# Performance work log

Measured on AMD Instinct MI355X. Metric: run time of the kernel, lower is better.

The kernel has to match this reference:

```python
import jax, jax.numpy as jnp
import numpy as np

STRIDE = (1, 2, 2, 1)

def setup_inputs() -> dict:
    key = jax.random.key(0)
    k1, k2 = jax.random.split(key)
    B, H, W, C = 8, 128, 128, 64
    out_flat = (H * STRIDE[1]) * (W * STRIDE[2]) * C  # 4194304
    inputs = jax.random.normal(k1, (B, H, W, C), dtype=jnp.float32)
    indices = jax.random.randint(k2, (B, H, W, C), 0, out_flat, dtype=jnp.int64)
    return {"inputs": inputs, "indices": indices}

def reference(inputs, indices):
    # Max-unpooling: scatter pooled values into a (stride_h*H, stride_w*W) map
    # using per-batch flat argmax indices. tf.scatter_nd sums duplicates -> .add
    B, H, W, C = inputs.shape
    oH, oW = H * STRIDE[1], W * STRIDE[2]
    flat_out = oH * oW * C
    pool_flat = inputs.reshape(B, H * W * C)
    ind_flat = indices.reshape(B, H * W * C)
    b = jnp.arange(B, dtype=ind_flat.dtype)[:, None]  # [B,1] batch index
    ret = jnp.zeros((B, flat_out), dtype=inputs.dtype)
    ret = ret.at[jnp.broadcast_to(b, ind_flat.shape), ind_flat].add(pool_flat)
    return ret.reshape(B, oH, oW, C)
```

## Files before the change

### kernel.cpp

```cpp
#include <hip/hip_runtime.h>


typedef unsigned int u32;
typedef float nat_f4 __attribute__((ext_vector_type(4)));

constexpr int N             = 1 << 23;
constexpr int NBINS         = 4096;
constexpr int BINS_PER_B    = 512;
constexpr int BIN_FLOATS    = 8192;
constexpr int CAP           = 3072;
constexpr int KA_BLOCKS     = 1024;
constexpr int PAIRS_PER_BLK = 8192;
constexpr size_t SLAB_BYTES = (size_t)NBINS * CAP * 8;
constexpr size_t WS_NEEDED  = SLAB_BYTES + (size_t)NBINS * 4;

__global__ __launch_bounds__(512, 4) void kA_sort(const int4* __restrict__ idx4,
                                                  const float4* __restrict__ val4,
                                                  uint2* __restrict__ slab,
                                                  u32* __restrict__ cursor) {
    __shared__ u32 lhist[BINS_PER_B];
    __shared__ u32 lstart[BINS_PER_B];
    __shared__ u32 lbase[BINS_PER_B];
    __shared__ u32 wsum[8];
    __shared__ uint2 sorted[PAIRS_PER_BLK];

    const int tid = threadIdx.x;
    lhist[tid] = 0;
    __syncthreads();

    const int cb4 = blockIdx.x * (PAIRS_PER_BLK / 4);
    const u32 bb  = (u32)(blockIdx.x >> 7) << 9;

    int4   ix[4];
    float4 vv[4];
    u32    rr[16];
#pragma unroll
    for (int i = 0; i < 4; ++i) {
        ix[i] = idx4[cb4 + i * 512 + tid];
        vv[i] = val4[cb4 + i * 512 + tid];
    }
#pragma unroll
    for (int i = 0; i < 4; ++i) {
        rr[4 * i + 0] = atomicAdd(&lhist[(u32)ix[i].x >> 13], 1u);
        rr[4 * i + 1] = atomicAdd(&lhist[(u32)ix[i].y >> 13], 1u);
        rr[4 * i + 2] = atomicAdd(&lhist[(u32)ix[i].z >> 13], 1u);
        rr[4 * i + 3] = atomicAdd(&lhist[(u32)ix[i].w >> 13], 1u);
    }
    __syncthreads();

    const int lane = tid & 63, w = tid >> 6;
    const u32 v = lhist[tid];
    u32 s = v;
#pragma unroll
    for (int d = 1; d < 64; d <<= 1) {
        u32 t = __shfl_up(s, d);
        if (lane >= d) s += t;
    }
    if (lane == 63) wsum[w] = s;
    __syncthreads();
    if (tid == 0) {
        u32 acc = 0;
#pragma unroll
        for (int i = 0; i < 8; ++i) { u32 t = wsum[i]; wsum[i] = acc; acc += t; }
    }
    __syncthreads();
    lstart[tid] = s - v + wsum[w];
    lbase[tid] = v ? atomicAdd(&cursor[bb + tid], v) : 0u;
    __syncthreads();

#pragma unroll
    for (int i = 0; i < 4; ++i) {
        sorted[lstart[(u32)ix[i].x >> 13] + rr[4 * i + 0]] =
            make_uint2(__float_as_uint(vv[i].x), (u32)ix[i].x);
        sorted[lstart[(u32)ix[i].y >> 13] + rr[4 * i + 1]] =
            make_uint2(__float_as_uint(vv[i].y), (u32)ix[i].y);
        sorted[lstart[(u32)ix[i].z >> 13] + rr[4 * i + 2]] =
            make_uint2(__float_as_uint(vv[i].z), (u32)ix[i].z);
        sorted[lstart[(u32)ix[i].w >> 13] + rr[4 * i + 3]] =
            make_uint2(__float_as_uint(vv[i].w), (u32)ix[i].w);
    }
    __syncthreads();

#pragma unroll
    for (int k = 0; k < 16; ++k) {
        int j = k * 512 + tid;
        uint2 p = sorted[j];
        u32 b = p.y >> 13;
        u32 r = lbase[b] + ((u32)j - lstart[b]);
        if (r < (u32)CAP)
            slab[(size_t)(bb + b) * CAP + r] = make_uint2(p.x, p.y & 8191u);
    }
}

__global__ __launch_bounds__(512) void kB_accum(const uint2* __restrict__ slab,
                                                const u32* __restrict__ cursor,
                                                float* __restrict__ out) {
    __shared__ float acc[BIN_FLOATS];
    const int bin = blockIdx.x, tid = threadIdx.x;

    nat_f4* a4 = (nat_f4*)acc;
#pragma unroll
    for (int i = 0; i < 4; ++i) a4[tid + i * 512] = (nat_f4)0.f;
    u32 cnt = cursor[bin];
    if (cnt > (u32)CAP) cnt = (u32)CAP;
    const uint2* seg = slab + (size_t)bin * CAP;
    __syncthreads();

    const uint4* seg4 = (const uint4*)seg;
    const u32 half = cnt >> 1;
    for (u32 j = tid; j < half; j += 512) {
        uint4 p = seg4[j];
        atomicAdd(&acc[p.y], __uint_as_float(p.x));
        atomicAdd(&acc[p.w], __uint_as_float(p.z));
    }
    if (tid == 0 && (cnt & 1u)) {
        uint2 p = seg[cnt - 1];
        atomicAdd(&acc[p.y], __uint_as_float(p.x));
    }
    __syncthreads();

    nat_f4* o4 = (nat_f4*)(out + ((size_t)bin << 13));
#pragma unroll
    for (int i = 0; i < 4; ++i)
        __builtin_nontemporal_store(a4[tid + i * 512], &o4[tid + i * 512]);
}

__global__ __launch_bounds__(256) void zero_out(float4* __restrict__ out) {
    int t = blockIdx.x * blockDim.x + threadIdx.x;
    out[t] = make_float4(0.f, 0.f, 0.f, 0.f);
}
__global__ __launch_bounds__(256) void scatter_atomic(const float4* __restrict__ in,
                                                      const int4* __restrict__ idx,
                                                      float* __restrict__ out) {
    int t = blockIdx.x * blockDim.x + threadIdx.x;
    float4 v = in[t];
    int4 ix = idx[t];
    float* obase = out + ((size_t)(t >> 18) << 22);
    atomicAdd(obase + ix.x, v.x);
    atomicAdd(obase + ix.y, v.y);
    atomicAdd(obase + ix.z, v.z);
    atomicAdd(obase + ix.w, v.w);
}

extern "C" void kernel_launch(void* const* d_in, const int* in_sizes, int n_in,
                              void* d_out, int out_size, void* d_ws, size_t ws_size,
                              hipStream_t stream) {
    const float4* val4 = (const float4*)d_in[0];
    const int4*   idx4 = (const int4*)d_in[1];
    float*        out  = (float*)d_out;

    if (ws_size < WS_NEEDED) {
        zero_out<<<(out_size / 4) / 256, 256, 0, stream>>>((float4*)d_out);
        scatter_atomic<<<(N / 4) / 256, 256, 0, stream>>>(val4, idx4, out);
        return;
    }

    uint2* slab   = (uint2*)d_ws;
    u32*   cursor = (u32*)((char*)d_ws + SLAB_BYTES);

    (void)hipMemsetAsync(cursor, 0, NBINS * sizeof(u32), stream);
    kA_sort <<<KA_BLOCKS, 512, 0, stream>>>(idx4, val4, slab, cursor);
    kB_accum<<<NBINS, 512, 0, stream>>>(slab, cursor, out);
}
```

Measured before the change: 250.3 us.

## Use 1024-thread sort blocks, nontemporal loads, and pad bin segments to multiples of eight

The sort kernel now runs 1024 threads per block, with each thread handling 8 pairs instead of 16, and reads its inputs with nontemporal loads. Each block reserves space in a bin segment rounded up to a multiple of eight entries and fills the padding with zero-value pairs. That keeps every block's chunk aligned and lets the accumulate kernel drop its odd-count tail handling. In exchange it writes extra padding entries and adds __syncthreads calls inside divergent branches. The padding also uses more of the fixed per-bin capacity, so overflow becomes more likely.

```diff
diff --git a/kernel.cpp b/kernel.cpp
--- a/kernel.cpp
+++ b/kernel.cpp
@@ -3,6 +3,7 @@
 
 typedef unsigned int u32;
 typedef float nat_f4 __attribute__((ext_vector_type(4)));
+typedef u32   nat_u4 __attribute__((ext_vector_type(4)));
 
 constexpr int N             = 1 << 23;
 constexpr int NBINS         = 4096;
@@ -14,10 +15,10 @@
 constexpr size_t SLAB_BYTES = (size_t)NBINS * CAP * 8;
 constexpr size_t WS_NEEDED  = SLAB_BYTES + (size_t)NBINS * 4;
 
-__global__ __launch_bounds__(512, 4) void kA_sort(const int4* __restrict__ idx4,
-                                                  const float4* __restrict__ val4,
-                                                  uint2* __restrict__ slab,
-                                                  u32* __restrict__ cursor) {
+__global__ __launch_bounds__(1024, 8) void kA_sort(const nat_u4* __restrict__ idx4,
+                                                   const nat_f4* __restrict__ val4,
+                                                   uint2* __restrict__ slab,
+                                                   u32* __restrict__ cursor) {
     __shared__ u32 lhist[BINS_PER_B];
     __shared__ u32 lstart[BINS_PER_B];
     __shared__ u32 lbase[BINS_PER_B];
@@ -25,70 +26,78 @@
     __shared__ uint2 sorted[PAIRS_PER_BLK];
 
     const int tid = threadIdx.x;
-    lhist[tid] = 0;
+    if (tid < BINS_PER_B) lhist[tid] = 0;
     __syncthreads();
 
     const int cb4 = blockIdx.x * (PAIRS_PER_BLK / 4);
     const u32 bb  = (u32)(blockIdx.x >> 7) << 9;
 
-    int4   ix[4];
-    float4 vv[4];
-    u32    rr[16];
+    nat_u4 ix[2];
+    nat_f4 vv[2];
+    u32    rr[8];
 #pragma unroll
-    for (int i = 0; i < 4; ++i) {
-        ix[i] = idx4[cb4 + i * 512 + tid];
-        vv[i] = val4[cb4 + i * 512 + tid];
+    for (int i = 0; i < 2; ++i) {
+        ix[i] = __builtin_nontemporal_load(&idx4[cb4 + i * 1024 + tid]);
+        vv[i] = __builtin_nontemporal_load(&val4[cb4 + i * 1024 + tid]);
     }
 #pragma unroll
-    for (int i = 0; i < 4; ++i) {
-        rr[4 * i + 0] = atomicAdd(&lhist[(u32)ix[i].x >> 13], 1u);
-        rr[4 * i + 1] = atomicAdd(&lhist[(u32)ix[i].y >> 13], 1u);
-        rr[4 * i + 2] = atomicAdd(&lhist[(u32)ix[i].z >> 13], 1u);
-        rr[4 * i + 3] = atomicAdd(&lhist[(u32)ix[i].w >> 13], 1u);
-    }
+    for (int i = 0; i < 2; ++i)
+#pragma unroll
+        for (int c = 0; c < 4; ++c)
+            rr[4 * i + c] = atomicAdd(&lhist[ix[i][c] >> 13], 1u);
     __syncthreads();
 
-    const int lane = tid & 63, w = tid >> 6;
-    const u32 v = lhist[tid];
-    u32 s = v;
+    if (tid < BINS_PER_B) {
+        const int lane = tid & 63, w = tid >> 6;
+        const u32 v = lhist[tid];
+        u32 s = v;
 #pragma unroll
-    for (int d = 1; d < 64; d <<= 1) {
-        u32 t = __shfl_up(s, d);
-        if (lane >= d) s += t;
-    }
-    if (lane == 63) wsum[w] = s;
-    __syncthreads();
-    if (tid == 0) {
-        u32 acc = 0;
+        for (int d = 1; d < 64; d <<= 1) {
+            u32 t = __shfl_up(s, d);
+            if (lane >= d) s += t;
+        }
+        if (lane == 63) wsum[w] = s;
+        __syncthreads();
+        if (tid == 0) {
+            u32 acc = 0;
 #pragma unroll
-        for (int i = 0; i < 8; ++i) { u32 t = wsum[i]; wsum[i] = acc; acc += t; }
-    }
-    __syncthreads();
-    lstart[tid] = s - v + wsum[w];
-    lbase[tid] = v ? atomicAdd(&cursor[bb + tid], v) : 0u;
-    __syncthreads();
-
-#pragma unroll
-    for (int i = 0; i < 4; ++i) {
-        sorted[lstart[(u32)ix[i].x >> 13] + rr[4 * i + 0]] =
-            make_uint2(__float_as_uint(vv[i].x), (u32)ix[i].x);
-        sorted[lstart[(u32)ix[i].y >> 13] + rr[4 * i + 1]] =
-            make_uint2(__float_as_uint(vv[i].y), (u32)ix[i].y);
-        sorted[lstart[(u32)ix[i].z >> 13] + rr[4 * i + 2]] =
-            make_uint2(__float_as_uint(vv[i].z), (u32)ix[i].z);
-        sorted[lstart[(u32)ix[i].w >> 13] + rr[4 * i + 3]] =
-            make_uint2(__float_as_uint(vv[i].w), (u32)ix[i].w);
+            for (int i = 0; i < 8; ++i) { u32 t = wsum[i]; wsum[i] = acc; acc += t; }
+        }
+        __syncthreads();
+        lstart[tid] = s - v + wsum[w];
+        const u32 r8 = (v + 7u) & ~7u;
+        lbase[tid] = r8 ? atomicAdd(&cursor[bb + tid], r8) : 0u;
+    } else {
+        __syncthreads();
+        __syncthreads();
     }
     __syncthreads();
 
 #pragma unroll
-    for (int k = 0; k < 16; ++k) {
-        int j = k * 512 + tid;
+    for (int i = 0; i < 2; ++i)
+#pragma unroll
+        for (int c = 0; c < 4; ++c)
+            sorted[lstart[ix[i][c] >> 13] + rr[4 * i + c]] =
+                make_uint2(__float_as_uint(vv[i][c]), ix[i][c]);
+    __syncthreads();
+
+#pragma unroll
+    for (int k = 0; k < 8; ++k) {
+        int j = k * 1024 + tid;
         uint2 p = sorted[j];
         u32 b = p.y >> 13;
         u32 r = lbase[b] + ((u32)j - lstart[b]);
         if (r < (u32)CAP)
             slab[(size_t)(bb + b) * CAP + r] = make_uint2(p.x, p.y & 8191u);
+    }
+    if (tid < BINS_PER_B) {
+        const u32 v = lhist[tid];
+        const u32 r8 = (v + 7u) & ~7u;
+        uint2* sb = slab + (size_t)(bb + tid) * CAP;
+        for (u32 q = v; q < r8; ++q) {
+            u32 r = lbase[tid] + q;
+            if (r < (u32)CAP) sb[r] = make_uint2(0u, 0u);
+        }
     }
 }
 
@@ -103,19 +112,14 @@
     for (int i = 0; i < 4; ++i) a4[tid + i * 512] = (nat_f4)0.f;
     u32 cnt = cursor[bin];
     if (cnt > (u32)CAP) cnt = (u32)CAP;
-    const uint2* seg = slab + (size_t)bin * CAP;
+    const uint4* seg4 = (const uint4*)(slab + (size_t)bin * CAP);
     __syncthreads();
 
-    const uint4* seg4 = (const uint4*)seg;
     const u32 half = cnt >> 1;
     for (u32 j = tid; j < half; j += 512) {
         uint4 p = seg4[j];
         atomicAdd(&acc[p.y], __uint_as_float(p.x));
         atomicAdd(&acc[p.w], __uint_as_float(p.z));
-    }
-    if (tid == 0 && (cnt & 1u)) {
-        uint2 p = seg[cnt - 1];
-        atomicAdd(&acc[p.y], __uint_as_float(p.x));
     }
     __syncthreads();
 
@@ -159,6 +163,7 @@
     u32*   cursor = (u32*)((char*)d_ws + SLAB_BYTES);
 
     (void)hipMemsetAsync(cursor, 0, NBINS * sizeof(u32), stream);
-    kA_sort <<<KA_BLOCKS, 512, 0, stream>>>(idx4, val4, slab, cursor);
+    kA_sort <<<KA_BLOCKS, 1024, 0, stream>>>((const nat_u4*)idx4, (const nat_f4*)val4,
+                                             slab, cursor);
     kB_accum<<<NBINS, 512, 0, stream>>>(slab, cursor, out);
 }
```

New measurement: 256.8 us. 1.03x slower.
